# Optimization experiments

Measured on AMD Instinct MI355X. Metric: run time of the kernel, lower is better.

The kernel has to match this reference:

```python
import jax, jax.numpy as jnp
from jax import lax
import numpy as np

L = 10          # number of integration steps
B, H, W = 4, 256, 256
HID = 100       # res_block hidden channels
SIGMA = 4.0     # RKHS Gaussian sigma
KSIZE = 25      # Gaussian kernel taps (~6*sigma+1, odd)
MU = 0.02       # residual weighting
SLOPE = 0.01    # LeakyReLU negative slope


def _conv(x, w, padding):
    return lax.conv_general_dilated(x, w, (1, 1), padding,
                                    dimension_numbers=('NCHW', 'OIHW', 'NCHW'))


def _sobel(img):
    # kornia SpatialGradient(mode='sobel'), normalized (L1 norm 8), replicate pad
    sx = jnp.array([[-1., 0., 1.], [-2., 0., 2.], [-1., 0., 1.]], img.dtype) / 8.0
    k = jnp.stack([sx, sx.T])[:, None]                     # [2,1,3,3] -> (dx, dy)
    imp = jnp.pad(img, ((0, 0), (0, 0), (1, 1), (1, 1)), mode='edge')
    return _conv(imp, k, 'VALID')                          # [B,2,H,W]


def _blur(x):
    # GaussianRKHS2d: separable normalized Gaussian, constant(zero) border
    b, c, h, w = x.shape
    r = jnp.arange(KSIZE, dtype=x.dtype) - (KSIZE - 1) / 2
    g = jnp.exp(-0.5 * (r / SIGMA) ** 2)
    g = g / jnp.sum(g)
    p = KSIZE // 2
    xr = x.reshape(b * c, 1, h, w)
    y = _conv(xr, g.reshape(1, 1, KSIZE, 1), [(p, p), (0, 0)])
    y = _conv(y, g.reshape(1, 1, 1, KSIZE), [(0, 0), (p, p)])
    return y.reshape(b, c, h, w)


def _deform(img, grid):
    # grid_sample(bilinear, zeros padding, align_corners=True) with pixel-coord grid (x,y)
    b, c, h, w = img.shape
    x = grid[..., 0]
    y = grid[..., 1]
    x0 = jnp.floor(x)
    y0 = jnp.floor(y)
    wx = x - x0
    wy = y - y0
    ix0 = x0.astype(jnp.int32)
    iy0 = y0.astype(jnp.int32)

    def samp(im, ix0, iy0, wx, wy):
        imf = im.reshape(c, h * w)

        def g(iy, ix):
            valid = ((ix >= 0) & (ix < w) & (iy >= 0) & (iy < h)).astype(im.dtype)
            idx = (jnp.clip(iy, 0, h - 1) * w + jnp.clip(ix, 0, w - 1)).reshape(-1)
            return imf[:, idx].reshape(c, h, w) * valid

        return (g(iy0, ix0) * (1 - wx) * (1 - wy)
                + g(iy0, ix0 + 1) * wx * (1 - wy)
                + g(iy0 + 1, ix0) * (1 - wx) * wy
                + g(iy0 + 1, ix0 + 1) * wx * wy)

    return jax.vmap(samp)(img, ix0, iy0, wx, wy)


def _res_block(z, img, w1, b1, w2):
    x = jnp.concatenate([z, img], axis=1)                  # [B,2,H,W]
    x = _conv(x, w1, 'SAME') + b1[None, :, None, None]
    x = jnp.where(x >= 0, x, SLOPE * x)                    # LeakyReLU
    return _conv(x, w2, 'SAME')                            # [B,1,H,W]


def _id_grid(b, dtype):
    gx, gy = jnp.meshgrid(jnp.arange(W, dtype=dtype), jnp.arange(H, dtype=dtype))
    g = jnp.stack([gx, gy], -1)                            # [H,W,2] (x,y) pixel coords
    return jnp.broadcast_to(g, (b, H, W, 2))


def _forward(source, source_seg, z0, w1, b1, w2):
    b = source.shape[0]
    idg = _id_grid(b, source.dtype)
    image = source
    res0 = jnp.broadcast_to(z0, (b,) + z0.shape[1:])       # [B,1,H,W]
    residuals = [res0]
    rd = res0                                              # residuals_deformed stacked on channel dim
    phi = idg
    fields, grads = [], []
    for i in range(L):
        g2 = _sobel(image)                                 # [B,2,H,W]
        grads.append(g2[:, None])                          # [B,1,2,H,W]
        field = _blur(-residuals[i] * g2).transpose(0, 2, 3, 1)  # [B,H,W,2]
        fields.append(field)
        deformation = idg - field / L
        f = _res_block(residuals[i], image, w1[i], b1[i], w2[i]) / L
        residuals.append(residuals[i] + f)
        rd = _deform(rd, deformation)                      # warp ALL previous residuals
        rd = jnp.concatenate([rd, residuals[-1]], axis=1)
        phi = _deform(phi.transpose(0, 3, 1, 2), deformation).transpose(0, 2, 3, 1)
        mask = _deform(source_seg, phi)
        image = _deform(source, phi) + jnp.sum(rd[:, 1:], axis=1, keepdims=True) * (MU ** 2 / L) * mask
    return image, jnp.stack(fields), jnp.stack(residuals), jnp.stack(grads)


def setup_inputs():
    key = jax.random.key(0)
    ks = jax.random.split(key, 5)
    source = jax.random.uniform(ks[0], (B, 1, H, W), jnp.float32)
    source_seg = jax.random.uniform(ks[1], (B, 1, H, W), jnp.float32)
    z0 = jax.random.normal(ks[2], (1, 1, H, W), jnp.float32) * 0.1
    w1 = jax.random.normal(ks[3], (L, HID, 2, 3, 3), jnp.float32) * 0.1
    b1 = jnp.zeros((L, HID), jnp.float32)
    w2 = jax.random.normal(ks[4], (L, 1, HID, 3, 3), jnp.float32) * 0.1
    return {"source": source, "source_seg": source_seg, "z0": z0,
            "w1": w1, "b1": b1, "w2": w2}


def reference(source, source_seg, z0, w1, b1, w2):
    return _forward(source, source_seg, z0, w1, b1, w2)
```

## Files before the change

kernel.cpp:

```cpp
#include <hip/hip_runtime.h>
#include <math.h>

#define L 10
#define B 4
#define H 256
#define W 256
#define HID 100
#define SIGMA 4.0f
#define KSIZE 25
#define KHALF 12
#define MU 0.02f
#define SLOPE 0.01f
#define HW (H*W)


__device__ __forceinline__ float tap2(const float* __restrict__ im, int y, int x) {
    return (x >= 0 && x < W && y >= 0 && y < H) ? im[y * W + x] : 0.f;
}

__device__ __forceinline__ float bilin(const float* __restrict__ im, float x, float y) {
    float xf = floorf(x), yf = floorf(y);
    int x0 = (int)xf, y0 = (int)yf;
    float wx = x - xf, wy = y - yf;
    float v00 = tap2(im, y0, x0),     v01 = tap2(im, y0, x0 + 1);
    float v10 = tap2(im, y0 + 1, x0), v11 = tap2(im, y0 + 1, x0 + 1);
    return v00 * (1.f - wx) * (1.f - wy) + v01 * wx * (1.f - wy)
         + v10 * (1.f - wx) * wy         + v11 * wx * wy;
}

__device__ __forceinline__ void gaussw(float g[KSIZE]) {
    float s = 0.f;
#pragma unroll
    for (int k = 0; k < KSIZE; ++k) {
        float r = ((float)k - (float)KHALF) * (1.f / SIGMA);
        float v = expf(-0.5f * r * r);
        g[k] = v; s += v;
    }
    float inv = 1.f / s;
#pragma unroll
    for (int k = 0; k < KSIZE; ++k) g[k] *= inv;
}


__global__ void init_kernel(const float* __restrict__ source, const float* __restrict__ z0,
                            float* __restrict__ res0_out, float* __restrict__ rd0,
                            float* __restrict__ phi0, float* __restrict__ image_buf) {
    int idx = blockIdx.x * 256 + threadIdx.x;
    if (idx >= B * HW) return;
    int b = idx / HW, p = idx % HW;
    int y = p / W, x = p % W;
    float z = z0[p];
    res0_out[idx] = z;
    rd0[(size_t)(b * 11 + 0) * HW + p] = z;
    image_buf[idx] = source[idx];
    phi0[(size_t)(b * 2 + 0) * HW + p] = (float)x;
    phi0[(size_t)(b * 2 + 1) * HW + p] = (float)y;
}


__global__ __launch_bounds__(256)
void field_kernel(const float* __restrict__ img, const float* __restrict__ res,
                  float* __restrict__ grads_l, float* __restrict__ field_l) {
    __shared__ float s_img[58][59];
    __shared__ float s_t[2][56][57];
    __shared__ float s_vb[2][32][57];

    const int tid = threadIdx.x;
    const int b = blockIdx.z;
    const int TY0 = blockIdx.y * 32, TX0 = blockIdx.x * 32;
    const float* imb = img + (size_t)b * HW;
    const float* reb = res + (size_t)b * HW;

    for (int q = tid; q < 58 * 58; q += 256) {
        int sy = q / 58, sx = q % 58;
        int gy = min(max(TY0 - 13 + sy, 0), H - 1);
        int gx = min(max(TX0 - 13 + sx, 0), W - 1);
        s_img[sy][sx] = imb[gy * W + gx];
    }
    __syncthreads();

    for (int q = tid; q < 56 * 56; q += 256) {
        int py = q / 56, px = q % 56;
        int sy = py + 1, sx = px + 1;
        float a00 = s_img[sy-1][sx-1], a01 = s_img[sy-1][sx], a02 = s_img[sy-1][sx+1];
        float a10 = s_img[sy  ][sx-1],                         a12 = s_img[sy  ][sx+1];
        float a20 = s_img[sy+1][sx-1], a21 = s_img[sy+1][sx], a22 = s_img[sy+1][sx+1];
        float dx = (a02 - a00 + 2.f * (a12 - a10) + a22 - a20) * 0.125f;
        float dy = (a20 - a00 + 2.f * (a21 - a01) + a22 - a02) * 0.125f;
        int gy = TY0 - 12 + py, gx = TX0 - 12 + px;
        bool in = ((unsigned)gy < H) && ((unsigned)gx < W);
        float rv = in ? reb[gy * W + gx] : 0.f;
        s_t[0][py][px] = in ? -rv * dx : 0.f;
        s_t[1][py][px] = in ? -rv * dy : 0.f;
        if (py >= 12 && py < 44 && px >= 12 && px < 44) {
            grads_l[(size_t)(b * 2 + 0) * HW + gy * W + gx] = dx;
            grads_l[(size_t)(b * 2 + 1) * HW + gy * W + gx] = dy;
        }
    }
    __syncthreads();

    float g[KSIZE]; gaussw(g);

    for (int q = tid; q < 2 * 32 * 56; q += 256) {
        int ch = q / (32 * 56), r = q % (32 * 56);
        int vy = r / 56, vx = r % 56;
        float acc = 0.f;
#pragma unroll
        for (int k = 0; k < KSIZE; ++k) acc = fmaf(g[k], s_t[ch][vy + k][vx], acc);
        s_vb[ch][vy][vx] = acc;
    }
    __syncthreads();

    for (int q = tid; q < 2 * 32 * 32; q += 256) {
        int ch = q / 1024, p = q % 1024;
        int hy = p / 32, hx = p % 32;
        float acc = 0.f;
#pragma unroll
        for (int k = 0; k < KSIZE; ++k) acc = fmaf(g[k], s_vb[ch][hy][hx + k], acc);
        field_l[((size_t)(b * H + TY0 + hy) * W + TX0 + hx) * 2 + ch] = acc;
    }
}


__global__ __launch_bounds__(256, 4)
void resblock_kernel(const float* __restrict__ res_i, const float* __restrict__ img,
                     const float* __restrict__ w1, const float* __restrict__ b1,
                     const float* __restrict__ w2, float* __restrict__ part) {
    __shared__ float s_in[2][20][21];
    __shared__ float s_T[9][324];

    const int tid = threadIdx.x;
    const int z = blockIdx.z;
    const int b = z & 3;
    const int g = z >> 2;
    const int TY0 = blockIdx.y * 16, TX0 = blockIdx.x * 16;

    for (int q = tid; q < 20 * 20; q += 256) {
        int ry = q / 20, rx = q % 20;
        int gy = TY0 - 2 + ry, gx = TX0 - 2 + rx;
        bool v = ((unsigned)gy < H) && ((unsigned)gx < W);
        size_t gp = (size_t)b * HW + gy * W + gx;
        s_in[0][ry][rx] = v ? res_i[gp] : 0.f;
        s_in[1][ry][rx] = v ? img[gp]   : 0.f;
    }
    __syncthreads();

    const int qq  = (tid < 162) ? tid : 161;
    const int hy  = qq / 9, hx2 = (qq % 9) * 2;
    const int gy1 = TY0 - 1 + hy, gx0 = TX0 - 1 + hx2;
    const bool gyok = ((unsigned)gy1 < H);
    const bool in0 = gyok && ((unsigned)gx0 < W);
    const bool in1 = gyok && ((unsigned)(gx0 + 1) < W);

    float xv[2][3][4];
#pragma unroll
    for (int ic = 0; ic < 2; ++ic)
#pragma unroll
        for (int j = 0; j < 3; ++j)
#pragma unroll
            for (int i = 0; i < 4; ++i)
                xv[ic][j][i] = s_in[ic][hy + j][hx2 + i];

    float T0[9], T1[9];
#pragma unroll
    for (int t = 0; t < 9; ++t) { T0[t] = 0.f; T1[t] = 0.f; }

#pragma unroll 1
    for (int cp = 0; cp < 25; ++cp) {
        const int chA = g * 50 + cp * 2;
        const float* wpA = w1 + chA * 18;
        const float* wpB = wpA + 18;
        float bA = b1[chA], bB = b1[chA + 1];
        float a0 = bA, a1 = bA, c0 = bB, c1 = bB;
#pragma unroll
        for (int ic = 0; ic < 2; ++ic)
#pragma unroll
            for (int j = 0; j < 3; ++j)
#pragma unroll
                for (int i = 0; i < 3; ++i) {
                    float wA = wpA[ic * 9 + j * 3 + i];
                    float wB = wpB[ic * 9 + j * 3 + i];
                    a0 = fmaf(wA, xv[ic][j][i],     a0);
                    a1 = fmaf(wA, xv[ic][j][i + 1], a1);
                    c0 = fmaf(wB, xv[ic][j][i],     c0);
                    c1 = fmaf(wB, xv[ic][j][i + 1], c1);
                }
        a0 = (a0 >= 0.f) ? a0 : SLOPE * a0;
        a1 = (a1 >= 0.f) ? a1 : SLOPE * a1;
        c0 = (c0 >= 0.f) ? c0 : SLOPE * c0;
        c1 = (c1 >= 0.f) ? c1 : SLOPE * c1;
        a0 = in0 ? a0 : 0.f;  c0 = in0 ? c0 : 0.f;
        a1 = in1 ? a1 : 0.f;  c1 = in1 ? c1 : 0.f;
        const float* wqA = w2 + chA * 9;
        const float* wqB = wqA + 9;
#pragma unroll
        for (int t = 0; t < 9; ++t) {
            float vA = wqA[t], vB = wqB[t];
            T0[t] = fmaf(vA, a0, T0[t]);
            T0[t] = fmaf(vB, c0, T0[t]);
            T1[t] = fmaf(vA, a1, T1[t]);
            T1[t] = fmaf(vB, c1, T1[t]);
        }
    }

    if (tid < 162) {
        const int pos = hy * 18 + hx2;
#pragma unroll
        for (int t = 0; t < 9; ++t) {
            float2 wv; wv.x = T0[t]; wv.y = T1[t];
            *(float2*)&s_T[t][pos] = wv;
        }
    }
    __syncthreads();

    const int ty = tid >> 4, tx = tid & 15;
    float acc = 0.f;
#pragma unroll
    for (int j = 0; j < 3; ++j)
#pragma unroll
        for (int i = 0; i < 3; ++i)
            acc += s_T[j * 3 + i][(ty + j) * 18 + (tx + i)];

    size_t gp = (size_t)b * HW + (TY0 + ty) * W + TX0 + tx;
    part[(size_t)g * (B * HW) + gp] = acc;
}


__global__ void efg_kernel(const float* __restrict__ field,
                           const float* __restrict__ res_prev,
                           const float* __restrict__ part,
                           float* __restrict__ res_next,
                           const float* __restrict__ rd_old, float* __restrict__ rd_new,
                           int nc_old,
                           const float* __restrict__ phi_old, float* __restrict__ phi_new,
                           const float* __restrict__ seg, const float* __restrict__ source,
                           float* __restrict__ image_buf, float* __restrict__ image_out) {
    int idx = blockIdx.x * 256 + threadIdx.x;
    if (idx >= B * HW) return;
    int b = idx / HW, p = idx % HW;
    int y = p / W, x = p % W;

    float rn = res_prev[idx] + (part[idx] + part[(size_t)B * HW + idx]) * (1.f / (float)L);
    res_next[idx] = rn;

    float fx = field[((size_t)(b * HW + p)) * 2 + 0];
    float fy = field[((size_t)(b * HW + p)) * 2 + 1];
    float sx = (float)x - fx * (1.f / (float)L);
    float sy = (float)y - fy * (1.f / (float)L);

    float xf = floorf(sx), yf = floorf(sy);
    int x0 = (int)xf, y0 = (int)yf;
    float wx = sx - xf, wy = sy - yf;
    float mx0 = (x0 >= 0 && x0 < W) ? 1.f : 0.f;
    float mx1 = (x0 + 1 >= 0 && x0 + 1 < W) ? 1.f : 0.f;
    float my0 = (y0 >= 0 && y0 < H) ? 1.f : 0.f;
    float my1 = (y0 + 1 >= 0 && y0 + 1 < H) ? 1.f : 0.f;
    float W00 = (1.f - wx) * (1.f - wy) * mx0 * my0;
    float W01 = wx * (1.f - wy) * mx1 * my0;
    float W10 = (1.f - wx) * wy * mx0 * my1;
    float W11 = wx * wy * mx1 * my1;
    int xc0 = min(max(x0, 0), W - 1), xc1 = min(max(x0 + 1, 0), W - 1);
    int yc0 = min(max(y0, 0), H - 1), yc1 = min(max(y0 + 1, 0), H - 1);
    int o00 = yc0 * W + xc0, o01 = yc0 * W + xc1;
    int o10 = yc1 * W + xc0, o11 = yc1 * W + xc1;

    float s = 0.f;
    for (int c = 0; c < nc_old; ++c) {
        const float* im = rd_old + (size_t)(b * 11 + c) * HW;
        float v = W00 * im[o00] + W01 * im[o01] + W10 * im[o10] + W11 * im[o11];
        rd_new[(size_t)(b * 11 + c) * HW + p] = v;
        if (c > 0) s += v;
    }
    rd_new[(size_t)(b * 11 + nc_old) * HW + p] = rn;
    s += rn;

    const float* phx = phi_old + (size_t)(b * 2 + 0) * HW;
    const float* phy = phi_old + (size_t)(b * 2 + 1) * HW;
    float pxn = W00 * phx[o00] + W01 * phx[o01] + W10 * phx[o10] + W11 * phx[o11];
    float pyn = W00 * phy[o00] + W01 * phy[o01] + W10 * phy[o10] + W11 * phy[o11];
    phi_new[(size_t)(b * 2 + 0) * HW + p] = pxn;
    phi_new[(size_t)(b * 2 + 1) * HW + p] = pyn;

    float mask = bilin(seg + (size_t)b * HW, pxn, pyn);
    float sw   = bilin(source + (size_t)b * HW, pxn, pyn);
    float img = sw + s * (MU * MU / (float)L) * mask;
    image_buf[idx] = img;
    image_out[idx] = img;
}


extern "C" void kernel_launch(void* const* d_in, const int* in_sizes, int n_in,
                              void* d_out, int out_size, void* d_ws, size_t ws_size,
                              hipStream_t stream) {
    const float* source = (const float*)d_in[0];
    const float* seg    = (const float*)d_in[1];
    const float* z0     = (const float*)d_in[2];
    const float* w1     = (const float*)d_in[3];
    const float* b1     = (const float*)d_in[4];
    const float* w2     = (const float*)d_in[5];
    float* out = (float*)d_out;

    const size_t nPix = (size_t)B * HW;
    float* out_image  = out;
    float* out_fields = out + nPix;
    float* out_res    = out_fields + (size_t)L * nPix * 2;
    float* out_grads  = out_res + (size_t)(L + 1) * nPix;

    float* ws        = (float*)d_ws;
    float* image_buf = ws;
    float* part_buf  = image_buf + nPix;
    float* phi_buf0  = part_buf + 2 * nPix;
    float* phi_buf1  = phi_buf0 + 2 * nPix;
    float* rd_buf0   = phi_buf1 + 2 * nPix;
    float* rd_buf1   = rd_buf0 + 11 * nPix;
    float* phi_buf[2] = { phi_buf0, phi_buf1 };
    float* rd_buf[2]  = { rd_buf0, rd_buf1 };

    dim3 blk(256);
    int gPix = (int)((nPix + 255) / 256);

    init_kernel<<<gPix, blk, 0, stream>>>(source, z0, out_res, rd_buf[0], phi_buf[0], image_buf);

    int cur = 0;
    for (int i = 0; i < L; ++i) {
        dim3 gF(W / 32, H / 32, B);
        field_kernel<<<gF, 256, 0, stream>>>(image_buf, out_res + (size_t)i * nPix,
                                             out_grads + (size_t)i * 2 * nPix,
                                             out_fields + (size_t)i * 2 * nPix);
        dim3 gD(W / 16, H / 16, 2 * B);
        resblock_kernel<<<gD, 256, 0, stream>>>(out_res + (size_t)i * nPix, image_buf,
                                                w1 + (size_t)i * HID * 18,
                                                b1 + (size_t)i * HID,
                                                w2 + (size_t)i * HID * 9,
                                                part_buf);
        efg_kernel<<<gPix, blk, 0, stream>>>(out_fields + (size_t)i * 2 * nPix,
                                             out_res + (size_t)i * nPix,
                                             part_buf,
                                             out_res + (size_t)(i + 1) * nPix,
                                             rd_buf[cur], rd_buf[cur ^ 1], i + 1,
                                             phi_buf[cur], phi_buf[cur ^ 1],
                                             seg, source, image_buf, out_image);
        cur ^= 1;
    }
}
```

Before: 595.3 us.

## Remap resblock to one hidden pixel per thread with 14x14 output tiles

```diff
diff --git a/kernel.cpp b/kernel.cpp
--- a/kernel.cpp
+++ b/kernel.cpp
@@ -122,21 +122,21 @@
 }
 
 
-__global__ __launch_bounds__(256, 4)
+__global__ __launch_bounds__(256, 8)
 void resblock_kernel(const float* __restrict__ res_i, const float* __restrict__ img,
                      const float* __restrict__ w1, const float* __restrict__ b1,
                      const float* __restrict__ w2, float* __restrict__ part) {
-    __shared__ float s_in[2][20][21];
-    __shared__ float s_T[9][324];
+    __shared__ float s_in[2][18][19];
+    __shared__ float s_T[9][256];
 
     const int tid = threadIdx.x;
     const int z = blockIdx.z;
     const int b = z & 3;
     const int g = z >> 2;
-    const int TY0 = blockIdx.y * 16, TX0 = blockIdx.x * 16;
-
-    for (int q = tid; q < 20 * 20; q += 256) {
-        int ry = q / 20, rx = q % 20;
+    const int TY0 = blockIdx.y * 14, TX0 = blockIdx.x * 14;
+
+    for (int q = tid; q < 18 * 18; q += 256) {
+        int ry = q / 18, rx = q % 18;
         int gy = TY0 - 2 + ry, gx = TX0 - 2 + rx;
         bool v = ((unsigned)gy < H) && ((unsigned)gx < W);
         size_t gp = (size_t)b * HW + gy * W + gx;
@@ -145,84 +145,68 @@
     }
     __syncthreads();
 
-    const int qq  = (tid < 162) ? tid : 161;
-    const int hy  = qq / 9, hx2 = (qq % 9) * 2;
-    const int gy1 = TY0 - 1 + hy, gx0 = TX0 - 1 + hx2;
-    const bool gyok = ((unsigned)gy1 < H);
-    const bool in0 = gyok && ((unsigned)gx0 < W);
-    const bool in1 = gyok && ((unsigned)(gx0 + 1) < W);
-
-    float xv[2][3][4];
+    const int hy = tid >> 4, hx = tid & 15;
+    const int gy1 = TY0 - 1 + hy, gx1 = TX0 - 1 + hx;
+    const bool inimg = ((unsigned)gy1 < H) && ((unsigned)gx1 < W);
+
+    float xv[2][3][3];
 #pragma unroll
     for (int ic = 0; ic < 2; ++ic)
 #pragma unroll
         for (int j = 0; j < 3; ++j)
 #pragma unroll
-            for (int i = 0; i < 4; ++i)
-                xv[ic][j][i] = s_in[ic][hy + j][hx2 + i];
-
-    float T0[9], T1[9];
-#pragma unroll
-    for (int t = 0; t < 9; ++t) { T0[t] = 0.f; T1[t] = 0.f; }
+            for (int i = 0; i < 3; ++i)
+                xv[ic][j][i] = s_in[ic][hy + j][hx + i];
+
+    float T[9];
+#pragma unroll
+    for (int t = 0; t < 9; ++t) T[t] = 0.f;
 
 #pragma unroll 1
     for (int cp = 0; cp < 25; ++cp) {
         const int chA = g * 50 + cp * 2;
         const float* wpA = w1 + chA * 18;
         const float* wpB = wpA + 18;
-        float bA = b1[chA], bB = b1[chA + 1];
-        float a0 = bA, a1 = bA, c0 = bB, c1 = bB;
+        float a = b1[chA], c = b1[chA + 1];
 #pragma unroll
         for (int ic = 0; ic < 2; ++ic)
 #pragma unroll
             for (int j = 0; j < 3; ++j)
 #pragma unroll
                 for (int i = 0; i < 3; ++i) {
-                    float wA = wpA[ic * 9 + j * 3 + i];
-                    float wB = wpB[ic * 9 + j * 3 + i];
-                    a0 = fmaf(wA, xv[ic][j][i],     a0);
-                    a1 = fmaf(wA, xv[ic][j][i + 1], a1);
-                    c0 = fmaf(wB, xv[ic][j][i],     c0);
-                    c1 = fmaf(wB, xv[ic][j][i + 1], c1);
+                    float xvv = xv[ic][j][i];
+                    a = fmaf(wpA[ic * 9 + j * 3 + i], xvv, a);
+                    c = fmaf(wpB[ic * 9 + j * 3 + i], xvv, c);
                 }
-        a0 = (a0 >= 0.f) ? a0 : SLOPE * a0;
-        a1 = (a1 >= 0.f) ? a1 : SLOPE * a1;
-        c0 = (c0 >= 0.f) ? c0 : SLOPE * c0;
-        c1 = (c1 >= 0.f) ? c1 : SLOPE * c1;
-        a0 = in0 ? a0 : 0.f;  c0 = in0 ? c0 : 0.f;
-        a1 = in1 ? a1 : 0.f;  c1 = in1 ? c1 : 0.f;
+        a = (a >= 0.f) ? a : SLOPE * a;
+        c = (c >= 0.f) ? c : SLOPE * c;
+        a = inimg ? a : 0.f;
+        c = inimg ? c : 0.f;
         const float* wqA = w2 + chA * 9;
         const float* wqB = wqA + 9;
 #pragma unroll
         for (int t = 0; t < 9; ++t) {
-            float vA = wqA[t], vB = wqB[t];
-            T0[t] = fmaf(vA, a0, T0[t]);
-            T0[t] = fmaf(vB, c0, T0[t]);
-            T1[t] = fmaf(vA, a1, T1[t]);
-            T1[t] = fmaf(vB, c1, T1[t]);
+            T[t] = fmaf(wqA[t], a, T[t]);
+            T[t] = fmaf(wqB[t], c, T[t]);
         }
     }
 
-    if (tid < 162) {
-        const int pos = hy * 18 + hx2;
-#pragma unroll
-        for (int t = 0; t < 9; ++t) {
-            float2 wv; wv.x = T0[t]; wv.y = T1[t];
-            *(float2*)&s_T[t][pos] = wv;
-        }
-    }
-    __syncthreads();
-
-    const int ty = tid >> 4, tx = tid & 15;
-    float acc = 0.f;
-#pragma unroll
-    for (int j = 0; j < 3; ++j)
-#pragma unroll
-        for (int i = 0; i < 3; ++i)
-            acc += s_T[j * 3 + i][(ty + j) * 18 + (tx + i)];
-
-    size_t gp = (size_t)b * HW + (TY0 + ty) * W + TX0 + tx;
-    part[(size_t)g * (B * HW) + gp] = acc;
+#pragma unroll
+    for (int t = 0; t < 9; ++t) s_T[t][tid] = T[t];
+    __syncthreads();
+
+    if (tid < 196) {
+        const int ty = tid / 14, tx = tid % 14;
+        float acc = 0.f;
+#pragma unroll
+        for (int j = 0; j < 3; ++j)
+#pragma unroll
+            for (int i = 0; i < 3; ++i)
+                acc += s_T[j * 3 + i][(ty + j) * 16 + (tx + i)];
+        const int Y = TY0 + ty, X = TX0 + tx;
+        if (Y < H && X < W)
+            part[(size_t)g * (B * HW) + (size_t)b * HW + Y * W + X] = acc;
+    }
 }
 
 
@@ -327,7 +311,7 @@
         field_kernel<<<gF, 256, 0, stream>>>(image_buf, out_res + (size_t)i * nPix,
                                              out_grads + (size_t)i * 2 * nPix,
                                              out_fields + (size_t)i * 2 * nPix);
-        dim3 gD(W / 16, H / 16, 2 * B);
+        dim3 gD((W + 13) / 14, (H + 13) / 14, 2 * B);
         resblock_kernel<<<gD, 256, 0, stream>>>(out_res + (size_t)i * nPix, image_buf,
                                                 w1 + (size_t)i * HID * 18,
                                                 b1 + (size_t)i * HID,
```

New measurement: 710.3 us. 1.19x slower.
